# Optimization experiments

Hardware: AMD Instinct MI355X
Metric: run time of the kernel (lower is better)

Reference implementation:

```python
import jax, jax.numpy as jnp
import numpy as np

B, C, H, W = 8, 64, 64, 64


def setup_inputs() -> dict:
    key = jax.random.key(0)
    ks = jax.random.split(key, 8)
    s = 1.0 / np.sqrt(C)  # keep logits in a reasonable range
    return {
        "x": jax.random.normal(ks[0], (B, C, H, W), dtype=jnp.float32),
        "Wf": jax.random.normal(ks[1], (C, C), dtype=jnp.float32) * s,
        "bf": jax.random.normal(ks[2], (C,), dtype=jnp.float32) * s,
        "Wg": jax.random.normal(ks[3], (C, C), dtype=jnp.float32) * s,
        "bg": jax.random.normal(ks[4], (C,), dtype=jnp.float32) * s,
        "Wh": jax.random.normal(ks[5], (C, C), dtype=jnp.float32) * s,
        "bh": jax.random.normal(ks[6], (C,), dtype=jnp.float32) * s,
        "gamma": jax.random.normal(ks[7], (1,), dtype=jnp.float32),
    }


def reference(x, Wf, bf, Wg, bg, Wh, bh, gamma):
    b, c, h, w = x.shape
    n = h * w
    xf = x.reshape(b, c, n)  # [B, C, N]
    # 1x1 convs == per-pixel channel GEMMs
    f = jnp.einsum("oc,bcn->bon", Wf, xf) + bf[None, :, None]  # [B, C, N]
    g = jnp.einsum("oc,bcn->bon", Wg, xf) + bg[None, :, None]
    hh = jnp.einsum("oc,bcn->bon", Wh, xf) + bh[None, :, None]
    # att_in[b, i, j] = f[b, :, i] . g[b, :, j]  (f_x permuted then bmm with g_x)
    att = jax.nn.softmax(jnp.einsum("bci,bcj->bij", f, g), axis=-1)  # [B, N, N]
    # torch.bmm(h_x, attention): out[b, c, j] = sum_i h[b, c, i] * att[b, i, j]
    out = jnp.einsum("bci,bij->bcj", hh, att).reshape(b, c, h, w)
    return gamma[0] * out + x
```

## Files before the change

kernel.cpp:

```cpp
#include <hip/hip_runtime.h>

#define BB 8
#define CC 64
#define NN 4096
#define JCH 8
#define LOG2E 1.4426950408889634f

typedef float f32x4  __attribute__((ext_vector_type(4)));
typedef float f32x16 __attribute__((ext_vector_type(16)));
typedef _Float16 half8_t __attribute__((ext_vector_type(8)));
typedef int int4v __attribute__((ext_vector_type(4)));
typedef unsigned uint2v __attribute__((ext_vector_type(2)));


__global__ __launch_bounds__(384, 6) void qkv_kernel(
    const float* __restrict__ x,
    const float* __restrict__ Wf, const float* __restrict__ bf,
    const float* __restrict__ Wg, const float* __restrict__ bg,
    const float* __restrict__ Wh, const float* __restrict__ bh,
    _Float16* __restrict__ fT, _Float16* __restrict__ gT,
    _Float16* __restrict__ hT)
{
    __shared__ float xbuf[64][36];

    const int tid  = threadIdx.x;
    const int lane = tid & 63;
    const int wv   = tid >> 6;
    const int l31  = lane & 31;
    const int q5   = lane >> 5;
    const int z    = wv >> 1;
    const int ot   = wv & 1;
    const int n0   = blockIdx.x * 32;
    const int b    = blockIdx.y;

    if (tid < 256) {
        const int row = tid >> 2;
        const int px4 = (tid & 3) * 8;
        const float* src = x + (size_t)(b * CC + row) * NN + n0 + px4;
        *(f32x4*)&xbuf[row][px4]     = *(const f32x4*)(src);
        *(f32x4*)&xbuf[row][px4 + 4] = *(const f32x4*)(src + 4);
    }
    __syncthreads();

    half8_t xf[4];
#pragma unroll
    for (int kc = 0; kc < 4; ++kc) {
        const int kb = kc * 16 + q5 * 8;
        int4v p;
#pragma unroll
        for (int h2 = 0; h2 < 4; ++h2) {
            p[h2] = __builtin_bit_cast(int, __builtin_amdgcn_cvt_pkrtz(
                xbuf[kb + h2 * 2][l31], xbuf[kb + h2 * 2 + 1][l31]));
        }
        xf[kc] = __builtin_bit_cast(half8_t, p);
    }

    const float* W    = (z == 0) ? Wf : ((z == 1) ? Wg : Wh);
    const float* bias = (z == 0) ? bf : ((z == 1) ? bg : bh);

    half8_t wf[4];
    {
        const float* wrow = W + (size_t)(ot * 32 + l31) * CC;
#pragma unroll
        for (int kc = 0; kc < 4; ++kc) {
            const f32x4 w0 = *(const f32x4*)(wrow + kc * 16 + q5 * 8);
            const f32x4 w1 = *(const f32x4*)(wrow + kc * 16 + q5 * 8 + 4);
            int4v p;
            p[0] = __builtin_bit_cast(int, __builtin_amdgcn_cvt_pkrtz(w0[0], w0[1]));
            p[1] = __builtin_bit_cast(int, __builtin_amdgcn_cvt_pkrtz(w0[2], w0[3]));
            p[2] = __builtin_bit_cast(int, __builtin_amdgcn_cvt_pkrtz(w1[0], w1[1]));
            p[3] = __builtin_bit_cast(int, __builtin_amdgcn_cvt_pkrtz(w1[2], w1[3]));
            wf[kc] = __builtin_bit_cast(half8_t, p);
        }
    }

    if (z < 2) {
        f32x16 acc = {};
#pragma unroll
        for (int kc = 0; kc < 4; ++kc)
            acc = __builtin_amdgcn_mfma_f32_32x32x16_f16(xf[kc], wf[kc], acc, 0, 0, 0);
        _Float16* dstT = (z == 0) ? fT : gT;
        const float scale = (z == 0) ? LOG2E : 1.0f;
        const float bv = bias[ot * 32 + l31];
#pragma unroll
        for (int r = 0; r < 16; ++r) {
            const int prow = (r & 3) + 8 * (r >> 2) + 4 * q5;
            dstT[(size_t)(b * NN + n0 + prow) * CC + ot * 32 + l31] =
                (_Float16)((acc[r] + bv) * scale);
        }
    } else {
        f32x16 acc = {};
#pragma unroll
        for (int kc = 0; kc < 4; ++kc)
            acc = __builtin_amdgcn_mfma_f32_32x32x16_f16(wf[kc], xf[kc], acc, 0, 0, 0);
        _Float16* hbase = hT + ((size_t)(b * (NN / 32) + blockIdx.x) * CC) * 32;
#pragma unroll
        for (int rb = 0; rb < 4; ++rb) {
            const f32x4 b4 = *(const f32x4*)(bias + ot * 32 + rb * 8 + q5 * 4);
#pragma unroll
            for (int k = 0; k < 4; ++k) {
                const int c = ot * 32 + rb * 8 + q5 * 4 + k;
                hbase[(size_t)c * 32 + l31] = (_Float16)(acc[rb * 4 + k] + b4[k]);
            }
        }
    }
}

__global__ __launch_bounds__(256, 4) void stats_kernel(
    const _Float16* __restrict__ fT, const _Float16* __restrict__ gT,
    float* __restrict__ lpart)
{
    __shared__ _Float16 gbuf[2][64][72];

    const int lane = threadIdx.x & 63;
    const int wv   = threadIdx.x >> 6;
    const int b    = blockIdx.y;
    const int jc   = blockIdx.z;
    const int i0   = blockIdx.x * 128 + wv * 32;
    const int l31  = lane & 31;
    const int q5   = lane >> 5;

    half8_t a[4];
    const _Float16* fa = fT + (size_t)(b * NN + i0 + l31) * CC + q5 * 8;
#pragma unroll
    for (int kc = 0; kc < 4; ++kc) a[kc] = *(const half8_t*)(fa + kc * 16);

    const _Float16* gchunk = gT + (size_t)(b * NN + jc * (NN / JCH)) * CC;
    const int T = NN / JCH / 64;

    const int srow = wv * 16 + (lane >> 3);
    const int scol = (lane & 7) * 8;

    {
        const half8_t v0 = *(const half8_t*)(gchunk + (size_t)srow * CC + scol);
        const half8_t v1 = *(const half8_t*)(gchunk + (size_t)(srow + 8) * CC + scol);
        *(half8_t*)&gbuf[0][srow][scol] = v0;
        *(half8_t*)&gbuf[0][srow + 8][scol] = v1;
    }
    __syncthreads();

    float l16[16];
#pragma unroll
    for (int r = 0; r < 16; ++r) l16[r] = 0.f;

    for (int t = 0; t < T; ++t) {
        const int buf = t & 1;
        const bool pf = (t + 1 < T);
        half8_t p0, p1;
        if (pf) {
            const _Float16* src = gchunk + (size_t)((t + 1) * 64 + srow) * CC + scol;
            p0 = *(const half8_t*)(src);
            p1 = *(const half8_t*)(src + 8 * CC);
        }
#pragma unroll
        for (int js = 0; js < 2; ++js) {
            const _Float16* grow = &gbuf[buf][js * 32 + l31][0] + q5 * 8;
            f32x16 s = {};
#pragma unroll
            for (int kc = 0; kc < 4; ++kc) {
                const half8_t bfr = *(const half8_t*)(grow + kc * 16);
                s = __builtin_amdgcn_mfma_f32_32x32x16_f16(a[kc], bfr, s, 0, 0, 0);
            }
#pragma unroll
            for (int r = 0; r < 16; ++r) l16[r] += __builtin_exp2f(s[r]);
        }
        if (pf) {
            *(half8_t*)&gbuf[buf ^ 1][srow][scol] = p0;
            *(half8_t*)&gbuf[buf ^ 1][srow + 8][scol] = p1;
        }
        __syncthreads();
    }

#pragma unroll
    for (int r = 0; r < 16; ++r) {
#pragma unroll
        for (int off = 1; off < 32; off <<= 1)
            l16[r] += __shfl_xor(l16[r], off);
    }

    if (l31 == 0) {
        float* lp = lpart + (size_t)jc * BB * NN + b * NN + i0;
#pragma unroll
        for (int rb = 0; rb < 4; ++rb) {
            f32x4 v;
#pragma unroll
            for (int k = 0; k < 4; ++k) v[k] = l16[rb * 4 + k];
            *(f32x4*)(lp + rb * 8 + q5 * 4) = v;
        }
    }
}

template <int NICT>
__global__ __launch_bounds__(256, 2) void attn_kernel(
    const _Float16* __restrict__ fT, const _Float16* __restrict__ gT,
    const _Float16* __restrict__ hT, const float* __restrict__ lpart,
    _Float16* __restrict__ pout)
{
    constexpr int ichunk = NN / NICT;
    __shared__ _Float16 fbuf[2][64][72];
    __shared__ _Float16 hbuf[2][64][72];
    __shared__ float nbbuf[ichunk];

    const int lane = threadIdx.x & 63;
    const int wv   = threadIdx.x >> 6;
    const int b    = blockIdx.y;
    const int ic   = blockIdx.z;
    const int l31  = lane & 31;
    const int q5   = lane >> 5;
    const int jbase = blockIdx.x * 256 + wv * 64;

    const int ibase  = ic * ichunk;
    const int tid    = threadIdx.x;

    if (tid * 4 < ichunk) {
        const float* lp0 = lpart + b * NN + ibase + tid * 4;
        f32x4 sum = *(const f32x4*)(lp0);
#pragma unroll
        for (int jc = 1; jc < JCH; ++jc) {
            const f32x4 v = *(const f32x4*)(lp0 + (size_t)jc * BB * NN);
#pragma unroll
            for (int k = 0; k < 4; ++k) sum[k] += v[k];
        }
        f32x4 nb4;
#pragma unroll
        for (int k = 0; k < 4; ++k) nb4[k] = -__builtin_log2f(sum[k]);
        *(f32x4*)&nbbuf[tid * 4] = nb4;
    }

    half8_t bg[2][4];
#pragma unroll
    for (int jt = 0; jt < 2; ++jt) {
        const _Float16* grow = gT + (size_t)(b * NN + jbase + jt * 32 + l31) * CC + q5 * 8;
#pragma unroll
        for (int kc = 0; kc < 4; ++kc) bg[jt][kc] = *(const half8_t*)(grow + kc * 16);
    }

    f32x16 acc[2][2] = {};

    const _Float16* fchunk = fT + ((size_t)b * NN + ibase) * CC;
    const _Float16* hchunk = hT + ((size_t)(b * (NN / 32) + ibase / 32) * CC) * 32;
    const int T = ichunk / 64;

    const int frow_s = tid >> 2;
    const int fcol_s = (tid & 3) * 16;
    const int hrow_s = tid >> 2;
    const int hcol_s = (tid & 3) * 8;

    {
        const half8_t f0 = *(const half8_t*)(fchunk + (size_t)frow_s * CC + fcol_s);
        const half8_t f1 = *(const half8_t*)(fchunk + (size_t)frow_s * CC + fcol_s + 8);
        const half8_t h0 = *(const half8_t*)(hchunk + tid * 8);
        const half8_t h1 = *(const half8_t*)(hchunk + 2048 + tid * 8);
        *(half8_t*)&fbuf[0][frow_s][fcol_s]     = f0;
        *(half8_t*)&fbuf[0][frow_s][fcol_s + 8] = f1;
        *(half8_t*)&hbuf[0][hrow_s][hcol_s]      = h0;
        *(half8_t*)&hbuf[0][hrow_s][32 + hcol_s] = h1;
    }
    __syncthreads();

    for (int t = 0; t < T; ++t) {
        const int buf = t & 1;
        const bool pf = (t + 1 < T);
        half8_t pf0, pf1, ph0, ph1;
        if (pf) {
            const _Float16* fsrc = fchunk + (size_t)((t + 1) * 64 + frow_s) * CC + fcol_s;
            const _Float16* hsrc = hchunk + (size_t)(t + 1) * 4096 + tid * 8;
            pf0 = *(const half8_t*)(fsrc);
            pf1 = *(const half8_t*)(fsrc + 8);
            ph0 = *(const half8_t*)(hsrc);
            ph1 = *(const half8_t*)(hsrc + 2048);
        }

        f32x16 s[2][2];
#pragma unroll
        for (int ih = 0; ih < 2; ++ih) {
            f32x16 si;
#pragma unroll
            for (int rb = 0; rb < 4; ++rb) {
                const f32x4 n4 = *(const f32x4*)&nbbuf[t * 64 + ih * 32 + rb * 8 + q5 * 4];
#pragma unroll
                for (int k = 0; k < 4; ++k) si[rb * 4 + k] = n4[k];
            }
            s[ih][0] = si;
            s[ih][1] = si;
        }
#pragma unroll
        for (int ih = 0; ih < 2; ++ih) {
            const _Float16* frow = &fbuf[buf][ih * 32 + l31][0] + q5 * 8;
#pragma unroll
            for (int kc = 0; kc < 4; ++kc) {
                const half8_t af = *(const half8_t*)(frow + kc * 16);
                s[ih][0] = __builtin_amdgcn_mfma_f32_32x32x16_f16(af, bg[0][kc], s[ih][0], 0, 0, 0);
                s[ih][1] = __builtin_amdgcn_mfma_f32_32x32x16_f16(af, bg[1][kc], s[ih][1], 0, 0, 0);
            }
        }

        half8_t B[2][2][2];
#pragma unroll
        for (int ih = 0; ih < 2; ++ih) {
#pragma unroll
            for (int jt = 0; jt < 2; ++jt) {
                const f32x16& sv = s[ih][jt];
                int e[8];
#pragma unroll
                for (int r8 = 0; r8 < 8; ++r8) {
                    e[r8] = __builtin_bit_cast(int, __builtin_amdgcn_cvt_pkrtz(
                        __builtin_exp2f(sv[r8 * 2]), __builtin_exp2f(sv[r8 * 2 + 1])));
                }
                int4v b0, b1;
#if __has_builtin(__builtin_amdgcn_permlane32_swap)
                const uint2v p02 = __builtin_amdgcn_permlane32_swap(
                    (unsigned)e[0], (unsigned)e[2], false, false);
                const uint2v p13 = __builtin_amdgcn_permlane32_swap(
                    (unsigned)e[1], (unsigned)e[3], false, false);
                const uint2v p46 = __builtin_amdgcn_permlane32_swap(
                    (unsigned)e[4], (unsigned)e[6], false, false);
                const uint2v p57 = __builtin_amdgcn_permlane32_swap(
                    (unsigned)e[5], (unsigned)e[7], false, false);
                b0[0] = (int)p02[0]; b0[1] = (int)p13[0];
                b0[2] = (int)p02[1]; b0[3] = (int)p13[1];
                b1[0] = (int)p46[0]; b1[1] = (int)p57[0];
                b1[2] = (int)p46[1]; b1[3] = (int)p57[1];
#else
                const int sA = q5 ? e[0] : e[2];
                const int sB = q5 ? e[1] : e[3];
                const int sC = q5 ? e[4] : e[6];
                const int sD = q5 ? e[5] : e[7];
                const int rA = __shfl_xor(sA, 32, 64);
                const int rB = __shfl_xor(sB, 32, 64);
                const int rC = __shfl_xor(sC, 32, 64);
                const int rD = __shfl_xor(sD, 32, 64);
                b0[0] = q5 ? rA   : e[0];
                b0[1] = q5 ? rB   : e[1];
                b0[2] = q5 ? e[2] : rA;
                b0[3] = q5 ? e[3] : rB;
                b1[0] = q5 ? rC   : e[4];
                b1[1] = q5 ? rD   : e[5];
                b1[2] = q5 ? e[6] : rC;
                b1[3] = q5 ? e[7] : rD;
#endif
                B[ih][jt][0] = __builtin_bit_cast(half8_t, b0);
                B[ih][jt][1] = __builtin_bit_cast(half8_t, b1);
            }
        }

#pragma unroll
        for (int ih = 0; ih < 2; ++ih) {
#pragma unroll
            for (int ct = 0; ct < 2; ++ct) {
                const half8_t ah0 = *(const half8_t*)(&hbuf[buf][ct * 32 + l31][0] + ih * 32 + q5 * 8);
                const half8_t ah1 = *(const half8_t*)(&hbuf[buf][ct * 32 + l31][0] + ih * 32 + 16 + q5 * 8);
                acc[0][ct] = __builtin_amdgcn_mfma_f32_32x32x16_f16(ah0, B[ih][0][0], acc[0][ct], 0, 0, 0);
                acc[0][ct] = __builtin_amdgcn_mfma_f32_32x32x16_f16(ah1, B[ih][0][1], acc[0][ct], 0, 0, 0);
                acc[1][ct] = __builtin_amdgcn_mfma_f32_32x32x16_f16(ah0, B[ih][1][0], acc[1][ct], 0, 0, 0);
                acc[1][ct] = __builtin_amdgcn_mfma_f32_32x32x16_f16(ah1, B[ih][1][1], acc[1][ct], 0, 0, 0);
            }
        }

        if (pf) {
            *(half8_t*)&fbuf[buf ^ 1][frow_s][fcol_s]     = pf0;
            *(half8_t*)&fbuf[buf ^ 1][frow_s][fcol_s + 8] = pf1;
            *(half8_t*)&hbuf[buf ^ 1][hrow_s][hcol_s]      = ph0;
            *(half8_t*)&hbuf[buf ^ 1][hrow_s][32 + hcol_s] = ph1;
        }
        __syncthreads();
    }

    _Float16* pb_out = pout + (((size_t)ic * BB + b) * CC) * NN;
#pragma unroll
    for (int jt = 0; jt < 2; ++jt) {
        const int j = jbase + jt * 32 + l31;
#pragma unroll
        for (int ct = 0; ct < 2; ++ct) {
#pragma unroll
            for (int r = 0; r < 16; ++r) {
                const int c = ct * 32 + (r & 3) + 8 * (r >> 2) + 4 * q5;
                pb_out[(size_t)c * NN + j] = (_Float16)acc[jt][ct][r];
            }
        }
    }
}

template <int NICT>
__global__ __launch_bounds__(256) void combine_kernel(
    const float* __restrict__ x, const float* __restrict__ gammap,
    const _Float16* __restrict__ pout, float* __restrict__ out)
{
    const float gam = gammap[0];
    const size_t i8 = ((size_t)blockIdx.x * 256 + threadIdx.x) * 8;
    const size_t TOT = (size_t)BB * CC * NN;

    float s[8] = {0.f, 0.f, 0.f, 0.f, 0.f, 0.f, 0.f, 0.f};
#pragma unroll
    for (int ic = 0; ic < NICT; ++ic) {
        const half8_t p = *(const half8_t*)(pout + ic * TOT + i8);
#pragma unroll
        for (int k = 0; k < 8; ++k) s[k] += (float)p[k];
    }
    const f32x4 x0 = *(const f32x4*)(x + i8);
    const f32x4 x1 = *(const f32x4*)(x + i8 + 4);
    f32x4 o0, o1;
#pragma unroll
    for (int k = 0; k < 4; ++k) { o0[k] = gam * s[k] + x0[k]; o1[k] = gam * s[k + 4] + x1[k]; }
    *(f32x4*)(out + i8) = o0;
    *(f32x4*)(out + i8 + 4) = o1;
}

extern "C" void kernel_launch(void* const* d_in, const int* in_sizes, int n_in,
                              void* d_out, int out_size, void* d_ws, size_t ws_size,
                              hipStream_t stream) {
    const float* x     = (const float*)d_in[0];
    const float* Wf    = (const float*)d_in[1];
    const float* bf    = (const float*)d_in[2];
    const float* Wg    = (const float*)d_in[3];
    const float* bg    = (const float*)d_in[4];
    const float* Wh    = (const float*)d_in[5];
    const float* bh    = (const float*)d_in[6];
    const float* gamma = (const float*)d_in[7];
    float* out = (float*)d_out;

    const size_t TOT = (size_t)BB * CC * NN;
    _Float16* fT   = (_Float16*)d_ws;
    _Float16* gT   = fT + TOT;
    _Float16* hT   = gT + TOT;
    _Float16* pout = hT + TOT;
    float* lpart   = (float*)(pout + (size_t)4 * TOT);

    qkv_kernel<<<dim3(NN / 32, BB), 384, 0, stream>>>(
        x, Wf, bf, Wg, bg, Wh, bh, fT, gT, hT);
    stats_kernel<<<dim3(NN / 128, BB, JCH), 256, 0, stream>>>(fT, gT, lpart);
    attn_kernel<4><<<dim3(NN / 256, BB, 4), 256, 0, stream>>>(fT, gT, hT, lpart, pout);
    combine_kernel<4><<<dim3(TOT / (256 * 8)), 256, 0, stream>>>(x, gamma, pout, out);
}
```

Before: 167.7 us.

## Process two i-tiles per barrier and raise wave priority around MFMA blocks

The attention loop now stages two 64-row tiles of f and h per double-buffer slot. Each iteration processes both tiles, which halves the number of __syncthreads barriers and doubles the prefetch batch in flight. s_setprio is raised around the MFMA sections so matrix work gets issue priority over other waves. In exchange, LDS use doubles (about 73KB plus nbbuf) and more prefetch registers are held, which may reduce occupancy below the 2 blocks per SM target.

```diff
diff --git a/kernel.cpp b/kernel.cpp
--- a/kernel.cpp
+++ b/kernel.cpp
@@ -197,8 +197,8 @@
     _Float16* __restrict__ pout)
 {
     constexpr int ichunk = NN / NICT;
-    __shared__ _Float16 fbuf[2][64][72];
-    __shared__ _Float16 hbuf[2][64][72];
+    __shared__ _Float16 fbuf[2][2][64][72];
+    __shared__ _Float16 hbuf[2][2][64][72];
     __shared__ float nbbuf[ichunk];
 
     const int lane = threadIdx.x & 63;
@@ -239,129 +239,144 @@
 
     const _Float16* fchunk = fT + ((size_t)b * NN + ibase) * CC;
     const _Float16* hchunk = hT + ((size_t)(b * (NN / 32) + ibase / 32) * CC) * 32;
-    const int T = ichunk / 64;
+    const int TP = (ichunk / 64) / 2;
 
     const int frow_s = tid >> 2;
     const int fcol_s = (tid & 3) * 16;
     const int hrow_s = tid >> 2;
     const int hcol_s = (tid & 3) * 8;
 
-    {
-        const half8_t f0 = *(const half8_t*)(fchunk + (size_t)frow_s * CC + fcol_s);
-        const half8_t f1 = *(const half8_t*)(fchunk + (size_t)frow_s * CC + fcol_s + 8);
-        const half8_t h0 = *(const half8_t*)(hchunk + tid * 8);
-        const half8_t h1 = *(const half8_t*)(hchunk + 2048 + tid * 8);
-        *(half8_t*)&fbuf[0][frow_s][fcol_s]     = f0;
-        *(half8_t*)&fbuf[0][frow_s][fcol_s + 8] = f1;
-        *(half8_t*)&hbuf[0][hrow_s][hcol_s]      = h0;
-        *(half8_t*)&hbuf[0][hrow_s][32 + hcol_s] = h1;
+#pragma unroll
+    for (int th = 0; th < 2; ++th) {
+        const _Float16* fsrc = fchunk + (size_t)(th * 64 + frow_s) * CC + fcol_s;
+        const _Float16* hsrc = hchunk + (size_t)th * 4096 + tid * 8;
+        *(half8_t*)&fbuf[0][th][frow_s][fcol_s]     = *(const half8_t*)(fsrc);
+        *(half8_t*)&fbuf[0][th][frow_s][fcol_s + 8] = *(const half8_t*)(fsrc + 8);
+        *(half8_t*)&hbuf[0][th][hrow_s][hcol_s]      = *(const half8_t*)(hsrc);
+        *(half8_t*)&hbuf[0][th][hrow_s][32 + hcol_s] = *(const half8_t*)(hsrc + 2048);
     }
     __syncthreads();
 
-    for (int t = 0; t < T; ++t) {
-        const int buf = t & 1;
-        const bool pf = (t + 1 < T);
-        half8_t pf0, pf1, ph0, ph1;
+    for (int tp = 0; tp < TP; ++tp) {
+        const int buf = tp & 1;
+        const bool pf = (tp + 1 < TP);
+        half8_t pf0[2], pf1[2], ph0[2], ph1[2];
         if (pf) {
-            const _Float16* fsrc = fchunk + (size_t)((t + 1) * 64 + frow_s) * CC + fcol_s;
-            const _Float16* hsrc = hchunk + (size_t)(t + 1) * 4096 + tid * 8;
-            pf0 = *(const half8_t*)(fsrc);
-            pf1 = *(const half8_t*)(fsrc + 8);
-            ph0 = *(const half8_t*)(hsrc);
-            ph1 = *(const half8_t*)(hsrc + 2048);
-        }
-
-        f32x16 s[2][2];
-#pragma unroll
-        for (int ih = 0; ih < 2; ++ih) {
-            f32x16 si;
-#pragma unroll
-            for (int rb = 0; rb < 4; ++rb) {
-                const f32x4 n4 = *(const f32x4*)&nbbuf[t * 64 + ih * 32 + rb * 8 + q5 * 4];
-#pragma unroll
-                for (int k = 0; k < 4; ++k) si[rb * 4 + k] = n4[k];
-            }
-            s[ih][0] = si;
-            s[ih][1] = si;
-        }
-#pragma unroll
-        for (int ih = 0; ih < 2; ++ih) {
-            const _Float16* frow = &fbuf[buf][ih * 32 + l31][0] + q5 * 8;
-#pragma unroll
-            for (int kc = 0; kc < 4; ++kc) {
-                const half8_t af = *(const half8_t*)(frow + kc * 16);
-                s[ih][0] = __builtin_amdgcn_mfma_f32_32x32x16_f16(af, bg[0][kc], s[ih][0], 0, 0, 0);
-                s[ih][1] = __builtin_amdgcn_mfma_f32_32x32x16_f16(af, bg[1][kc], s[ih][1], 0, 0, 0);
-            }
-        }
-
-        half8_t B[2][2][2];
-#pragma unroll
-        for (int ih = 0; ih < 2; ++ih) {
-#pragma unroll
-            for (int jt = 0; jt < 2; ++jt) {
-                const f32x16& sv = s[ih][jt];
-                int e[8];
-#pragma unroll
-                for (int r8 = 0; r8 < 8; ++r8) {
-                    e[r8] = __builtin_bit_cast(int, __builtin_amdgcn_cvt_pkrtz(
-                        __builtin_exp2f(sv[r8 * 2]), __builtin_exp2f(sv[r8 * 2 + 1])));
+#pragma unroll
+            for (int th = 0; th < 2; ++th) {
+                const int t = (tp + 1) * 2 + th;
+                const _Float16* fsrc = fchunk + (size_t)(t * 64 + frow_s) * CC + fcol_s;
+                const _Float16* hsrc = hchunk + (size_t)t * 4096 + tid * 8;
+                pf0[th] = *(const half8_t*)(fsrc);
+                pf1[th] = *(const half8_t*)(fsrc + 8);
+                ph0[th] = *(const half8_t*)(hsrc);
+                ph1[th] = *(const half8_t*)(hsrc + 2048);
+            }
+        }
+
+#pragma unroll
+        for (int th = 0; th < 2; ++th) {
+            const int t = tp * 2 + th;
+
+            f32x16 s[2][2];
+#pragma unroll
+            for (int ih = 0; ih < 2; ++ih) {
+                f32x16 si;
+#pragma unroll
+                for (int rb = 0; rb < 4; ++rb) {
+                    const f32x4 n4 = *(const f32x4*)&nbbuf[t * 64 + ih * 32 + rb * 8 + q5 * 4];
+#pragma unroll
+                    for (int k = 0; k < 4; ++k) si[rb * 4 + k] = n4[k];
                 }
-                int4v b0, b1;
+                s[ih][0] = si;
+                s[ih][1] = si;
+            }
+            __builtin_amdgcn_s_setprio(1);
+#pragma unroll
+            for (int ih = 0; ih < 2; ++ih) {
+                const _Float16* frow = &fbuf[buf][th][ih * 32 + l31][0] + q5 * 8;
+#pragma unroll
+                for (int kc = 0; kc < 4; ++kc) {
+                    const half8_t af = *(const half8_t*)(frow + kc * 16);
+                    s[ih][0] = __builtin_amdgcn_mfma_f32_32x32x16_f16(af, bg[0][kc], s[ih][0], 0, 0, 0);
+                    s[ih][1] = __builtin_amdgcn_mfma_f32_32x32x16_f16(af, bg[1][kc], s[ih][1], 0, 0, 0);
+                }
+            }
+            __builtin_amdgcn_s_setprio(0);
+
+            half8_t B[2][2][2];
+#pragma unroll
+            for (int ih = 0; ih < 2; ++ih) {
+#pragma unroll
+                for (int jt = 0; jt < 2; ++jt) {
+                    const f32x16& sv = s[ih][jt];
+                    int e[8];
+#pragma unroll
+                    for (int r8 = 0; r8 < 8; ++r8) {
+                        e[r8] = __builtin_bit_cast(int, __builtin_amdgcn_cvt_pkrtz(
+                            __builtin_exp2f(sv[r8 * 2]), __builtin_exp2f(sv[r8 * 2 + 1])));
+                    }
+                    int4v b0, b1;
 #if __has_builtin(__builtin_amdgcn_permlane32_swap)
-                const uint2v p02 = __builtin_amdgcn_permlane32_swap(
-                    (unsigned)e[0], (unsigned)e[2], false, false);
-                const uint2v p13 = __builtin_amdgcn_permlane32_swap(
-                    (unsigned)e[1], (unsigned)e[3], false, false);
-                const uint2v p46 = __builtin_amdgcn_permlane32_swap(
-                    (unsigned)e[4], (unsigned)e[6], false, false);
-                const uint2v p57 = __builtin_amdgcn_permlane32_swap(
-                    (unsigned)e[5], (unsigned)e[7], false, false);
-                b0[0] = (int)p02[0]; b0[1] = (int)p13[0];
-                b0[2] = (int)p02[1]; b0[3] = (int)p13[1];
-                b1[0] = (int)p46[0]; b1[1] = (int)p57[0];
-                b1[2] = (int)p46[1]; b1[3] = (int)p57[1];
+                    const uint2v p02 = __builtin_amdgcn_permlane32_swap(
+                        (unsigned)e[0], (unsigned)e[2], false, false);
+                    const uint2v p13 = __builtin_amdgcn_permlane32_swap(
+                        (unsigned)e[1], (unsigned)e[3], false, false);
+                    const uint2v p46 = __builtin_amdgcn_permlane32_swap(
+                        (unsigned)e[4], (unsigned)e[6], false, false);
+                    const uint2v p57 = __builtin_amdgcn_permlane32_swap(
+                        (unsigned)e[5], (unsigned)e[7], false, false);
+                    b0[0] = (int)p02[0]; b0[1] = (int)p13[0];
+                    b0[2] = (int)p02[1]; b0[3] = (int)p13[1];
+                    b1[0] = (int)p46[0]; b1[1] = (int)p57[0];
+                    b1[2] = (int)p46[1]; b1[3] = (int)p57[1];
 #else
-                const int sA = q5 ? e[0] : e[2];
-                const int sB = q5 ? e[1] : e[3];
-                const int sC = q5 ? e[4] : e[6];
-                const int sD = q5 ? e[5] : e[7];
-                const int rA = __shfl_xor(sA, 32, 64);
-                const int rB = __shfl_xor(sB, 32, 64);
-                const int rC = __shfl_xor(sC, 32, 64);
-                const int rD = __shfl_xor(sD, 32, 64);
-                b0[0] = q5 ? rA   : e[0];
-                b0[1] = q5 ? rB   : e[1];
-                b0[2] = q5 ? e[2] : rA;
-                b0[3] = q5 ? e[3] : rB;
-                b1[0] = q5 ? rC   : e[4];
-                b1[1] = q5 ? rD   : e[5];
-                b1[2] = q5 ? e[6] : rC;
-                b1[3] = q5 ? e[7] : rD;
+                    const int sA = q5 ? e[0] : e[2];
+                    const int sB = q5 ? e[1] : e[3];
+                    const int sC = q5 ? e[4] : e[6];
+                    const int sD = q5 ? e[5] : e[7];
+                    const int rA = __shfl_xor(sA, 32, 64);
+                    const int rB = __shfl_xor(sB, 32, 64);
+                    const int rC = __shfl_xor(sC, 32, 64);
+                    const int rD = __shfl_xor(sD, 32, 64);
+                    b0[0] = q5 ? rA   : e[0];
+                    b0[1] = q5 ? rB   : e[1];
+                    b0[2] = q5 ? e[2] : rA;
+                    b0[3] = q5 ? e[3] : rB;
+                    b1[0] = q5 ? rC   : e[4];
+                    b1[1] = q5 ? rD   : e[5];
+                    b1[2] = q5 ? e[6] : rC;
+                    b1[3] = q5 ? e[7] : rD;
 #endif
-                B[ih][jt][0] = __builtin_bit_cast(half8_t, b0);
-                B[ih][jt][1] = __builtin_bit_cast(half8_t, b1);
-            }
-        }
-
-#pragma unroll
-        for (int ih = 0; ih < 2; ++ih) {
-#pragma unroll
-            for (int ct = 0; ct < 2; ++ct) {
-                const half8_t ah0 = *(const half8_t*)(&hbuf[buf][ct * 32 + l31][0] + ih * 32 + q5 * 8);
-                const half8_t ah1 = *(const half8_t*)(&hbuf[buf][ct * 32 + l31][0] + ih * 32 + 16 + q5 * 8);
-                acc[0][ct] = __builtin_amdgcn_mfma_f32_32x32x16_f16(ah0, B[ih][0][0], acc[0][ct], 0, 0, 0);
-                acc[0][ct] = __builtin_amdgcn_mfma_f32_32x32x16_f16(ah1, B[ih][0][1], acc[0][ct], 0, 0, 0);
-                acc[1][ct] = __builtin_amdgcn_mfma_f32_32x32x16_f16(ah0, B[ih][1][0], acc[1][ct], 0, 0, 0);
-                acc[1][ct] = __builtin_amdgcn_mfma_f32_32x32x16_f16(ah1, B[ih][1][1], acc[1][ct], 0, 0, 0);
-            }
+                    B[ih][jt][0] = __builtin_bit_cast(half8_t, b0);
+                    B[ih][jt][1] = __builtin_bit_cast(half8_t, b1);
+                }
+            }
+
+            __builtin_amdgcn_s_setprio(1);
+#pragma unroll
+            for (int ih = 0; ih < 2; ++ih) {
+#pragma unroll
+                for (int ct = 0; ct < 2; ++ct) {
+                    const half8_t ah0 = *(const half8_t*)(&hbuf[buf][th][ct * 32 + l31][0] + ih * 32 + q5 * 8);
+                    const half8_t ah1 = *(const half8_t*)(&hbuf[buf][th][ct * 32 + l31][0] + ih * 32 + 16 + q5 * 8);
+                    acc[0][ct] = __builtin_amdgcn_mfma_f32_32x32x16_f16(ah0, B[ih][0][0], acc[0][ct], 0, 0, 0);
+                    acc[0][ct] = __builtin_amdgcn_mfma_f32_32x32x16_f16(ah1, B[ih][0][1], acc[0][ct], 0, 0, 0);
+                    acc[1][ct] = __builtin_amdgcn_mfma_f32_32x32x16_f16(ah0, B[ih][1][0], acc[1][ct], 0, 0, 0);
+                    acc[1][ct] = __builtin_amdgcn_mfma_f32_32x32x16_f16(ah1, B[ih][1][1], acc[1][ct], 0, 0, 0);
+                }
+            }
+            __builtin_amdgcn_s_setprio(0);
         }
 
         if (pf) {
-            *(half8_t*)&fbuf[buf ^ 1][frow_s][fcol_s]     = pf0;
-            *(half8_t*)&fbuf[buf ^ 1][frow_s][fcol_s + 8] = pf1;
-            *(half8_t*)&hbuf[buf ^ 1][hrow_s][hcol_s]      = ph0;
-            *(half8_t*)&hbuf[buf ^ 1][hrow_s][32 + hcol_s] = ph1;
+#pragma unroll
+            for (int th = 0; th < 2; ++th) {
+                *(half8_t*)&fbuf[buf ^ 1][th][frow_s][fcol_s]     = pf0[th];
+                *(half8_t*)&fbuf[buf ^ 1][th][frow_s][fcol_s + 8] = pf1[th];
+                *(half8_t*)&hbuf[buf ^ 1][th][hrow_s][hcol_s]      = ph0[th];
+                *(half8_t*)&hbuf[buf ^ 1][th][hrow_s][32 + hcol_s] = ph1[th];
+            }
         }
         __syncthreads();
     }
```

New measurement: 167.8 us (median of 2 runs). About the same (+0.1%).
